# Optimization experiments

Hardware: AMD Instinct MI355X
Metric: run time of the kernel (lower is better)

Reference implementation:

```python
import jax, jax.numpy as jnp
import numpy as np

EPS = 1e-7
DIM_PRIMARY = 8  # param.dim_primary_caps, used for attention_coef


def squash(v):
    # Squash (Mazzia et al. 2021): coef = 1 - exp(-||v||); unit = v / (||v|| + eps)
    norm = jnp.linalg.norm(v, axis=-1, keepdims=True)
    coef = 1.0 - 1.0 / jnp.exp(norm)
    return coef * v / (norm + EPS)


def setup_inputs() -> dict:
    key = jax.random.key(0)
    k1, k2, k3 = jax.random.split(key, 3)
    B, N, Dp = 16, 1152, 8   # batch, num_primary_caps, dim_primary_caps
    M, Dd = 10, 16           # num_digit_caps, dim_digit_caps
    primary_caps = jax.random.normal(k1, (B, N, Dp), dtype=jnp.float32)
    W = jax.random.normal(k2, (M, N, Dd, Dp), dtype=jnp.float32) * 0.05
    B_prior = jax.random.normal(k3, (M, 1, N), dtype=jnp.float32) * 0.05
    return {"primary_caps": primary_caps, "W": W, "B_prior": B_prior}


def reference(primary_caps, W, B_prior):
    coef = 1.0 / jnp.sqrt(jnp.float32(DIM_PRIMARY))
    # U_hat[b,m,n,d] = W[m,n,d,p] @ u[b,n,p]  (fused batched GEMM, replaces tf.map_fn)
    U_hat = jnp.einsum('mndp,bnp->bmnd', W, primary_caps)
    # attention scores A[b,m,n,k]
    A = coef * jnp.einsum('bmnd,bmkd->bmnk', U_hat, U_hat)
    # reduce over axis -2 (keepdims) then softmax over axis -2 (size-1 axis),
    # exactly as in the original code
    C = jax.nn.softmax(jnp.sum(A, axis=-2, keepdims=True), axis=-2)  # [b,m,1,n]
    CB = (C + B_prior[None])[:, :, 0, :]                             # [b,m,n]
    S = jnp.einsum('bmn,bmnd->bmd', CB, U_hat)                       # [b,m,d]
    return squash(S)
```

## Files before the change

### kernel.cpp

```cpp
#include <hip/hip_runtime.h>
#include <math.h>

#define BSZ   16
#define NCAPS 1152
#define DP    8
#define MCAPS 10
#define DD    16

#define NC     24
#define NCHUNK (NCAPS / NC)

__global__ __launch_bounds__(256) void digitcaps_partial(
    const float* __restrict__ u,
    const float* __restrict__ W,
    const float* __restrict__ Bp,
    float* __restrict__ S)
{
    __shared__ float w_t[NC][DD][DP];
    __shared__ float u_t[BSZ][NC][DP];
    __shared__ float bp_t[NC];

    const int t  = threadIdx.x;
    const int m  = blockIdx.x / NCHUNK;
    const int n0 = (blockIdx.x % NCHUNK) * NC;

    const float4* wg = (const float4*)(W + ((size_t)(m * NCAPS + n0)) * DD * DP);
    float4* wl = (float4*)&w_t[0][0][0];
#pragma unroll
    for (int i = 0; i < 3; ++i) {
        wl[t + 256 * i] = wg[t + 256 * i];
    }

    float4* ul = (float4*)&u_t[0][0][0];
#pragma unroll
    for (int i = 0; i < 3; ++i) {
        int idx = t + 256 * i;
        int b   = idx / (NC * DP / 4);
        int off = idx % (NC * DP / 4);
        ul[idx] = ((const float4*)(u + ((size_t)(b * NCAPS + n0)) * DP))[off];
    }

    if (t < NC) bp_t[t] = 1.0f + Bp[m * NCAPS + n0 + t];
    __syncthreads();

    const int b = t >> 4;
    const int d = t & 15;

    float acc = 0.0f;
#pragma unroll
    for (int n = 0; n < NC; ++n) {
        const float4 w0 = *(const float4*)&w_t[n][d][0];
        const float4 w1 = *(const float4*)&w_t[n][d][4];
        const float4 u0 = *(const float4*)&u_t[b][n][0];
        const float4 u1 = *(const float4*)&u_t[b][n][4];
        float dot = w0.x * u0.x + w0.y * u0.y + w0.z * u0.z + w0.w * u0.w
                  + w1.x * u1.x + w1.y * u1.y + w1.z * u1.z + w1.w * u1.w;
        acc += bp_t[n] * dot;
    }

    atomicAdd(&S[((size_t)b * MCAPS + m) * DD + d], acc);
}

__global__ __launch_bounds__(256) void digitcaps_squash(
    const float* __restrict__ S,
    float* __restrict__ out)
{
    const int t = threadIdx.x;
    if (t >= BSZ * MCAPS) return;

    const float* s = S + (size_t)t * DD;
    float v[DD];
    float ss = 0.0f;
#pragma unroll
    for (int d = 0; d < DD; ++d) {
        v[d] = s[d];
        ss += v[d] * v[d];
    }
    float norm  = sqrtf(ss);
    float coef  = 1.0f - expf(-norm);
    float scale = coef / (norm + 1e-7f);
#pragma unroll
    for (int d = 0; d < DD; ++d) {
        out[(size_t)t * DD + d] = scale * v[d];
    }
}

extern "C" void kernel_launch(void* const* d_in, const int* in_sizes, int n_in,
                              void* d_out, int out_size, void* d_ws, size_t ws_size,
                              hipStream_t stream) {
    const float* u  = (const float*)d_in[0];
    const float* W  = (const float*)d_in[1];
    const float* Bp = (const float*)d_in[2];
    float* out = (float*)d_out;
    float* S   = (float*)d_ws;

    hipMemsetAsync(S, 0, (size_t)BSZ * MCAPS * DD * sizeof(float), stream);

    digitcaps_partial<<<dim3(MCAPS * NCHUNK), dim3(256), 0, stream>>>(u, W, Bp, S);
    digitcaps_squash<<<dim3(1), dim3(256), 0, stream>>>(S, out);
}
```

Measured before the change: 67.30 us.

## Replace atomic accumulation and memset with per-block partials and fused reduce-squash

Each partial block now writes its per-(b,d) sums to a workspace slot instead of doing atomicAdd into S. A second kernel with 10 blocks sums the 48 chunk partials per output element, computes the norm through a width-16 shuffle reduction, and applies squash. This removes the memset launch and atomic contention on 2560 addresses. The cost is a larger workspace and a serial 48-load reduction per thread in the final kernel.

Result: no change. 66.60 us (-1.0%).

```diff
diff --git a/kernel.cpp b/kernel.cpp
--- a/kernel.cpp
+++ b/kernel.cpp
@@ -14,7 +14,7 @@
     const float* __restrict__ u,
     const float* __restrict__ W,
     const float* __restrict__ Bp,
-    float* __restrict__ S)
+    float* __restrict__ part)
 {
     __shared__ float w_t[NC][DD][DP];
     __shared__ float u_t[BSZ][NC][DP];
@@ -58,31 +58,34 @@
         acc += bp_t[n] * dot;
     }
 
-    atomicAdd(&S[((size_t)b * MCAPS + m) * DD + d], acc);
+    part[(size_t)blockIdx.x * 256 + t] = acc;
 }
 
-__global__ __launch_bounds__(256) void digitcaps_squash(
-    const float* __restrict__ S,
+__global__ __launch_bounds__(256) void digitcaps_reduce_squash(
+    const float* __restrict__ part,
     float* __restrict__ out)
 {
-    const int t = threadIdx.x;
-    if (t >= BSZ * MCAPS) return;
+    const int g  = blockIdx.x * 256 + threadIdx.x;
+    const int d  = g & 15;
+    const int bm = g >> 4;
+    const int m  = bm % MCAPS;
+    const int b  = bm / MCAPS;
 
-    const float* s = S + (size_t)t * DD;
-    float v[DD];
-    float ss = 0.0f;
+    float s = 0.0f;
 #pragma unroll
-    for (int d = 0; d < DD; ++d) {
-        v[d] = s[d];
-        ss += v[d] * v[d];
+    for (int c = 0; c < NCHUNK; ++c) {
+        s += part[(((size_t)(m * NCHUNK + c) * BSZ + b) << 4) + d];
     }
+
+    float ss = s * s;
+#pragma unroll
+    for (int w = 1; w < 16; w <<= 1) {
+        ss += __shfl_xor(ss, w, 16);
+    }
+
     float norm  = sqrtf(ss);
-    float coef  = 1.0f - expf(-norm);
-    float scale = coef / (norm + 1e-7f);
-#pragma unroll
-    for (int d = 0; d < DD; ++d) {
-        out[(size_t)t * DD + d] = scale * v[d];
-    }
+    float scale = (1.0f - expf(-norm)) / (norm + 1e-7f);
+    out[g] = scale * s;
 }
 
 extern "C" void kernel_launch(void* const* d_in, const int* in_sizes, int n_in,
@@ -91,11 +94,9 @@
     const float* u  = (const float*)d_in[0];
     const float* W  = (const float*)d_in[1];
     const float* Bp = (const float*)d_in[2];
-    float* out = (float*)d_out;
-    float* S   = (float*)d_ws;
+    float* out  = (float*)d_out;
+    float* part = (float*)d_ws;
 
-    hipMemsetAsync(S, 0, (size_t)BSZ * MCAPS * DD * sizeof(float), stream);
-
-    digitcaps_partial<<<dim3(MCAPS * NCHUNK), dim3(256), 0, stream>>>(u, W, Bp, S);
-    digitcaps_squash<<<dim3(1), dim3(256), 0, stream>>>(S, out);
+    digitcaps_partial<<<dim3(MCAPS * NCHUNK), dim3(256), 0, stream>>>(u, W, Bp, part);
+    digitcaps_reduce_squash<<<dim3(MCAPS), dim3(256), 0, stream>>>(part, out);
 }
```
